# Kernel optimization log

Measured on AMD Instinct MI355X. Metric: run time of the kernel, lower is better.

The kernel has to match this reference:

```python
import jax, jax.numpy as jnp
import numpy as np

B, S, E, H, D = 2, 2048, 1024, 16, 64  # batch, seq(=max_seq_len), embed_dim, heads, atten_dim


def setup_inputs() -> dict:
    key = jax.random.key(0)
    ks = jax.random.split(key, 9)
    s = 0.02
    return {
        "x": jax.random.normal(ks[0], (B, S, E), jnp.float32),
        "Wq": jax.random.normal(ks[1], (H, E, D), jnp.float32) * s,
        "Wk": jax.random.normal(ks[2], (H, E, D), jnp.float32) * s,
        "Wv": jax.random.normal(ks[3], (H, E, D), jnp.float32) * s,
        "bq": jax.random.normal(ks[4], (H, D), jnp.float32) * s,
        "bk": jax.random.normal(ks[5], (H, D), jnp.float32) * s,
        "bv": jax.random.normal(ks[6], (H, D), jnp.float32) * s,
        "Wp": jax.random.normal(ks[7], (H * D, E), jnp.float32) * s,
        "bp": jax.random.normal(ks[8], (E,), jnp.float32) * s,
    }


def reference(x, Wq, Wk, Wv, bq, bk, bv, Wp, bp):
    scale = jnp.sqrt(jnp.float32(D))
    # per-head projections, all heads at once: [B,H,S,D]
    q = jnp.einsum("bse,hed->bhsd", x, Wq) + bq[:, None, :]
    k = jnp.einsum("bse,hed->bhsd", x, Wk) + bk[:, None, :]
    v = jnp.einsum("bse,hed->bhsd", x, Wv) + bv[:, None, :]
    # causal scores [B,H,S,S], additive -inf mask above diagonal (as in the buffer)
    score = jnp.einsum("bhsd,bhtd->bhst", q, k) / scale
    mask = jnp.triu(jnp.full((S, S), -jnp.inf, jnp.float32), k=1)
    score = score + mask
    probs = jax.nn.softmax(score, axis=-1)
    attn = jnp.einsum("bhst,bhtd->bhsd", probs, v)
    # concat heads -> [B,S,H*D], then projection + ReLU
    concat = attn.transpose(0, 2, 1, 3).reshape(B, S, H * D)
    out = jax.nn.relu(concat @ Wp + bp)
    return out
```

## Files before the change

### kernel.cpp

```cpp
#include <hip/hip_runtime.h>

#define S_LEN 2048
#define E_DIM 1024
#define H_NUM 16
#define D_DIM 64

typedef unsigned short u16;
using bf16x8 = __attribute__((ext_vector_type(8))) short;
using f32x4  = __attribute__((ext_vector_type(4))) float;

#define MFMA16(A, B, C) __builtin_amdgcn_mfma_f32_16x16x32_bf16(A, B, C, 0, 0, 0)

__device__ __forceinline__ u16 f2bf(float f) {
    unsigned u = __float_as_uint(f);
    u += 0x7fffu + ((u >> 16) & 1u);
    return (u16)(u >> 16);
}
__device__ __forceinline__ f32x4 fzero4() { f32x4 z; z[0]=0.f; z[1]=0.f; z[2]=0.f; z[3]=0.f; return z; }

__device__ __forceinline__ void gll16(const u16* g, u16* l) {
    __builtin_amdgcn_global_load_lds(
        (const __attribute__((address_space(1))) void*)g,
        (__attribute__((address_space(3))) void*)l, 16, 0, 0);
}

__global__ __launch_bounds__(256) void cvt_bf16(const float* __restrict__ in, u16* __restrict__ outp, int n) {
    int i4 = (blockIdx.x * 256 + threadIdx.x) * 4;
    if (i4 < n) {
        float4 f = *(const float4*)(in + i4);
        unsigned lo = (unsigned)f2bf(f.x) | ((unsigned)f2bf(f.y) << 16);
        unsigned hi = (unsigned)f2bf(f.z) | ((unsigned)f2bf(f.w) << 16);
        uint2 p; p.x = lo; p.y = hi;
        *(uint2*)(outp + i4) = p;
    }
}

__device__ __forceinline__ void cvt_t_tile(const float* __restrict__ bin, u16* __restrict__ bout,
                                           int R, int C, int r0, int c0) {
    __shared__ float t[64][65];
    const int tid = threadIdx.x;
    const int lr = tid >> 2, lc = (tid & 3) * 16;

    const float* src = bin + (size_t)(r0 + lr) * C + c0 + lc;
    #pragma unroll
    for (int j = 0; j < 4; j++) {
        float4 f = *(const float4*)(src + j * 4);
        t[lr][lc + j * 4 + 0] = f.x; t[lr][lc + j * 4 + 1] = f.y;
        t[lr][lc + j * 4 + 2] = f.z; t[lr][lc + j * 4 + 3] = f.w;
    }
    __syncthreads();

    u16* dst = bout + (size_t)(c0 + lr) * R + r0 + lc;
    u16 vals[16];
    #pragma unroll
    for (int i = 0; i < 16; i++) vals[i] = f2bf(t[lc + i][lr]);
    uint4 pa, pb;
    pa.x = vals[0] | (vals[1] << 16);  pa.y = vals[2] | (vals[3] << 16);
    pa.z = vals[4] | (vals[5] << 16);  pa.w = vals[6] | (vals[7] << 16);
    pb.x = vals[8] | (vals[9] << 16);  pb.y = vals[10] | (vals[11] << 16);
    pb.z = vals[12] | (vals[13] << 16); pb.w = vals[14] | (vals[15] << 16);
    *(uint4*)dst = pa;
    *(uint4*)(dst + 8) = pb;
}

__global__ __launch_bounds__(256) void cvt_bf16_t(const float* __restrict__ in, u16* __restrict__ outp,
                                                  int R, int C) {
    const float* bin = in + (size_t)blockIdx.z * R * C;
    u16* bout = outp + (size_t)blockIdx.z * R * C;
    cvt_t_tile(bin, bout, R, C, blockIdx.y * 64, blockIdx.x * 64);
}

__global__ __launch_bounds__(256) void cvt_w3_t(
    const float* __restrict__ Wq, const float* __restrict__ Wk, const float* __restrict__ Wv,
    u16* __restrict__ wqt, u16* __restrict__ wkt, u16* __restrict__ wvt) {
    const int which = blockIdx.z >> 4, bh = blockIdx.z & 15;
    const float* in = (which == 0) ? Wq : (which == 1) ? Wk : Wv;
    u16* outp = (which == 0) ? wqt : (which == 1) ? wkt : wvt;
    const float* bin = in + (size_t)bh * E_DIM * D_DIM;
    u16* bout = outp + (size_t)bh * E_DIM * D_DIM;
    cvt_t_tile(bin, bout, E_DIM, D_DIM, blockIdx.y * 64, 0);
}

__global__ __launch_bounds__(256) void vt_prep(const u16* __restrict__ v, u16* __restrict__ vt) {
    const int st = blockIdx.x;
    const int bhi = blockIdx.y;
    __shared__ u16 t[64 * 72];
    const int tid = threadIdx.x;
    const int wave = tid >> 6, lane = tid & 63;

    const u16* src = v + (size_t)bhi * S_LEN * D_DIM + (size_t)(st * 64 + lane) * D_DIM + wave * 16;
    uint4 a = *(const uint4*)(src);
    uint4 b = *(const uint4*)(src + 8);
    unsigned w[8] = { a.x, a.y, a.z, a.w, b.x, b.y, b.z, b.w };
    #pragma unroll
    for (int j = 0; j < 8; j++) {
        t[(wave * 16 + 2 * j    ) * 72 + lane] = (u16)(w[j] & 0xffffu);
        t[(wave * 16 + 2 * j + 1) * 72 + lane] = (u16)(w[j] >> 16);
    }
    __syncthreads();

    const int dr = tid >> 2, sc = (tid & 3) * 16;
    u16* dst = vt + (size_t)bhi * D_DIM * S_LEN + (size_t)dr * S_LEN + st * 64 + sc;
    *(uint4*)(dst    ) = *(const uint4*)(&t[dr * 72 + sc    ]);
    *(uint4*)(dst + 8) = *(const uint4*)(&t[dr * 72 + sc + 8]);
}

__global__ __launch_bounds__(256) void qkv_gemm(
    const u16* __restrict__ xb, const u16* __restrict__ wcat,
    const float* __restrict__ bq, const float* __restrict__ bk, const float* __restrict__ bv,
    u16* __restrict__ oq, u16* __restrict__ okk, u16* __restrict__ ov)
{
    const int m0 = blockIdx.x * 128;
    const int n0 = blockIdx.y * 128;

    __shared__ u16 As[128 * 32];
    __shared__ u16 Bs[128 * 32];

    const int tid  = threadIdx.x;
    const int wave = tid >> 6, lane = tid & 63, quad = lane >> 4, l16 = lane & 15;
    const int mh = wave >> 1, nh = wave & 1;

    const int lrow = lane >> 2, lcol = (lane & 3) * 8;
    const u16* aBase = xb   + (size_t)(m0 + wave * 32 + lrow) * E_DIM + lcol;
    const u16* bBase = wcat + (size_t)(n0 + wave * 32 + lrow) * E_DIM + lcol;
    u16* aLds0 = &As[(wave * 32     ) * 32];
    u16* aLds1 = &As[(wave * 32 + 16) * 32];
    u16* bLds0 = &Bs[(wave * 32     ) * 32];
    u16* bLds1 = &Bs[(wave * 32 + 16) * 32];

    f32x4 acc[4][4];
    #pragma unroll
    for (int j = 0; j < 4; j++)
        #pragma unroll
        for (int mi = 0; mi < 4; mi++) acc[j][mi] = fzero4();

    for (int k0 = 0; k0 < E_DIM; k0 += 32) {
        __syncthreads();
        gll16(aBase + k0,                 aLds0);
        gll16(aBase + k0 + 16 * E_DIM,    aLds1);
        gll16(bBase + k0,                 bLds0);
        gll16(bBase + k0 + 16 * E_DIM,    bLds1);
        __syncthreads();

        bf16x8 af[4];
        #pragma unroll
        for (int mi = 0; mi < 4; mi++)
            af[mi] = *(const bf16x8*)(&As[(mh * 64 + mi * 16 + l16) * 32 + quad * 8]);
        #pragma unroll
        for (int j = 0; j < 4; j++) {
            bf16x8 bfv = *(const bf16x8*)(&Bs[(nh * 64 + j * 16 + l16) * 32 + quad * 8]);
            #pragma unroll
            for (int mi = 0; mi < 4; mi++)
                acc[j][mi] = MFMA16(af[mi], bfv, acc[j][mi]);
        }
    }

    u16* outp[3] = { oq, okk, ov };
    const float* biasp[3] = { bq, bk, bv };
    #pragma unroll
    for (int j = 0; j < 4; j++) {
        const int n = n0 + nh * 64 + j * 16 + l16;
        const int t = n >> 10, h = (n >> 6) & 15, d = n & 63;
        float bia = biasp[t][h * D_DIM + d];
        const float scl = (t == 0) ? 0.125f : 1.0f;
        u16* dst = outp[t];
        #pragma unroll
        for (int mi = 0; mi < 4; mi++) {
            #pragma unroll
            for (int r = 0; r < 4; r++) {
                int m = m0 + mh * 64 + mi * 16 + quad * 4 + r;
                int b = m >> 11, s = m & 2047;
                dst[((size_t)(b * H_NUM + h) * S_LEN + s) * D_DIM + d] =
                    f2bf((acc[j][mi][r] + bia) * scl);
            }
        }
    }
}

__global__ __launch_bounds__(256) void attn_fwd(
    const u16* __restrict__ q, const u16* __restrict__ k, const u16* __restrict__ vt,
    u16* __restrict__ concat)
{
    const int p  = blockIdx.x;
    const int qa = p, qb = 31 - p;
    const int h  = blockIdx.y;
    const int bb = blockIdx.z;

    const size_t headoff = (size_t)(bb * H_NUM + h) * S_LEN * D_DIM;
    const u16* qh  = q  + headoff;
    const u16* kh  = k  + headoff;
    const u16* vth = vt + headoff;

    __shared__ u16 Qa[64 * 72];
    __shared__ u16 Qb[64 * 72];
    __shared__ u16 Ks[64 * 72];
    __shared__ u16 Vts[64 * 72];
    __shared__ u16 Ps[4][16 * 72];

    const int tid  = threadIdx.x;
    const int wave = tid >> 6, lane = tid & 63, quad = lane >> 4, l16 = lane & 15;

    const int srow = tid >> 2, scg = tid & 3;

    {
        const u16* qsa = qh + (size_t)(qa * 64 + srow) * D_DIM + scg * 16;
        const u16* qsb = qh + (size_t)(qb * 64 + srow) * D_DIM + scg * 16;
        *(uint4*)(&Qa[srow * 72 + scg * 16    ]) = *(const uint4*)(qsa);
        *(uint4*)(&Qa[srow * 72 + scg * 16 + 8]) = *(const uint4*)(qsa + 8);
        *(uint4*)(&Qb[srow * 72 + scg * 16    ]) = *(const uint4*)(qsb);
        *(uint4*)(&Qb[srow * 72 + scg * 16 + 8]) = *(const uint4*)(qsb + 8);
    }
    __syncthreads();

    bf16x8 bqa0 = *(const bf16x8*)(&Qa[(wave * 16 + l16) * 72 + quad * 8]);
    bf16x8 bqa1 = *(const bf16x8*)(&Qa[(wave * 16 + l16) * 72 + 32 + quad * 8]);
    bf16x8 bqb0 = *(const bf16x8*)(&Qb[(wave * 16 + l16) * 72 + quad * 8]);
    bf16x8 bqb1 = *(const bf16x8*)(&Qb[(wave * 16 + l16) * 72 + 32 + quad * 8]);

    f32x4 oa[4], ob[4];
    #pragma unroll
    for (int nt = 0; nt < 4; nt++) { oa[nt] = fzero4(); ob[nt] = fzero4(); }
    float la = 0.f, lb = 0.f;

    uint4 kA, kB, vA, vB;
    {
        const u16* ksrc = kh + (size_t)srow * D_DIM + scg * 16;
        kA = *(const uint4*)(ksrc); kB = *(const uint4*)(ksrc + 8);
        const u16* vsrc = vth + (size_t)srow * S_LEN + scg * 16;
        vA = *(const uint4*)(vsrc); vB = *(const uint4*)(vsrc + 8);
    }

    const int qga = qa * 64 + wave * 16 + l16;
    const int qgb = qb * 64 + wave * 16 + l16;

    for (int kt = 0; kt <= qb; kt++) {
        __syncthreads();
        *(uint4*)(&Ks[srow * 72 + scg * 16    ]) = kA;
        *(uint4*)(&Ks[srow * 72 + scg * 16 + 8]) = kB;
        *(uint4*)(&Vts[srow * 72 + scg * 16    ]) = vA;
        *(uint4*)(&Vts[srow * 72 + scg * 16 + 8]) = vB;
        __syncthreads();

        if (kt < qb) {
            const u16* ksrc = kh + (size_t)((kt + 1) * 64 + srow) * D_DIM + scg * 16;
            kA = *(const uint4*)(ksrc); kB = *(const uint4*)(ksrc + 8);
            const u16* vsrc = vth + (size_t)srow * S_LEN + (kt + 1) * 64 + scg * 16;
            vA = *(const uint4*)(vsrc); vB = *(const uint4*)(vsrc + 8);
        }

        const bool both = (kt <= qa);

        f32x4 stb[4], sta[4];
        #pragma unroll
        for (int nt = 0; nt < 4; nt++) {
            bf16x8 ak0 = *(const bf16x8*)(&Ks[(nt * 16 + l16) * 72 + quad * 8]);
            bf16x8 ak1 = *(const bf16x8*)(&Ks[(nt * 16 + l16) * 72 + 32 + quad * 8]);
            stb[nt] = fzero4();
            stb[nt] = MFMA16(ak0, bqb0, stb[nt]);
            stb[nt] = MFMA16(ak1, bqb1, stb[nt]);
            if (both) {
                sta[nt] = fzero4();
                sta[nt] = MFMA16(ak0, bqa0, sta[nt]);
                sta[nt] = MFMA16(ak1, bqa1, sta[nt]);
            }
        }

        {
            u16* pw = &Ps[wave][0];
            #pragma unroll
            for (int nt = 0; nt < 4; nt++) {
                float pe[4];
                if (kt == qb) {
                    #pragma unroll
                    for (int r = 0; r < 4; r++) {
                        int kkg = kt * 64 + nt * 16 + quad * 4 + r;
                        pe[r] = (kkg > qgb) ? 0.f : __expf(stb[nt][r]);
                    }
                } else {
                    #pragma unroll
                    for (int r = 0; r < 4; r++) pe[r] = __expf(stb[nt][r]);
                }
                lb += pe[0] + pe[1] + pe[2] + pe[3];
                uint2 pk;
                pk.x = (unsigned)f2bf(pe[0]) | ((unsigned)f2bf(pe[1]) << 16);
                pk.y = (unsigned)f2bf(pe[2]) | ((unsigned)f2bf(pe[3]) << 16);
                *(uint2*)(&pw[l16 * 72 + nt * 16 + quad * 4]) = pk;
            }
            bf16x8 ap0 = *(const bf16x8*)(&Ps[wave][l16 * 72 + quad * 8]);
            bf16x8 ap1 = *(const bf16x8*)(&Ps[wave][l16 * 72 + 32 + quad * 8]);
            #pragma unroll
            for (int nt = 0; nt < 4; nt++) {
                bf16x8 bv0 = *(const bf16x8*)(&Vts[(nt * 16 + l16) * 72 + quad * 8]);
                bf16x8 bv1 = *(const bf16x8*)(&Vts[(nt * 16 + l16) * 72 + 32 + quad * 8]);
                ob[nt] = MFMA16(ap0, bv0, ob[nt]);
                ob[nt] = MFMA16(ap1, bv1, ob[nt]);
            }
        }

        if (both) {
            u16* pw = &Ps[wave][0];
            #pragma unroll
            for (int nt = 0; nt < 4; nt++) {
                float pe[4];
                if (kt == qa) {
                    #pragma unroll
                    for (int r = 0; r < 4; r++) {
                        int kkg = kt * 64 + nt * 16 + quad * 4 + r;
                        pe[r] = (kkg > qga) ? 0.f : __expf(sta[nt][r]);
                    }
                } else {
                    #pragma unroll
                    for (int r = 0; r < 4; r++) pe[r] = __expf(sta[nt][r]);
                }
                la += pe[0] + pe[1] + pe[2] + pe[3];
                uint2 pk;
                pk.x = (unsigned)f2bf(pe[0]) | ((unsigned)f2bf(pe[1]) << 16);
                pk.y = (unsigned)f2bf(pe[2]) | ((unsigned)f2bf(pe[3]) << 16);
                *(uint2*)(&pw[l16 * 72 + nt * 16 + quad * 4]) = pk;
            }
            bf16x8 ap0 = *(const bf16x8*)(&Ps[wave][l16 * 72 + quad * 8]);
            bf16x8 ap1 = *(const bf16x8*)(&Ps[wave][l16 * 72 + 32 + quad * 8]);
            #pragma unroll
            for (int nt = 0; nt < 4; nt++) {
                bf16x8 bv0 = *(const bf16x8*)(&Vts[(nt * 16 + l16) * 72 + quad * 8]);
                bf16x8 bv1 = *(const bf16x8*)(&Vts[(nt * 16 + l16) * 72 + 32 + quad * 8]);
                oa[nt] = MFMA16(ap0, bv0, oa[nt]);
                oa[nt] = MFMA16(ap1, bv1, oa[nt]);
            }
        }
    }

    lb += __shfl_xor(lb, 16); lb += __shfl_xor(lb, 32);
    la += __shfl_xor(la, 16); la += __shfl_xor(la, 32);

    #pragma unroll
    for (int r = 0; r < 4; r++) {
        const int srcl = quad * 4 + r;
        float lbr = __shfl(lb, srcl);
        float lar = __shfl(la, srcl);
        int sqa = qa * 64 + wave * 16 + quad * 4 + r;
        int sqb = qb * 64 + wave * 16 + quad * 4 + r;
        #pragma unroll
        for (int nt = 0; nt < 4; nt++) {
            concat[((size_t)(bb * S_LEN + sqa)) * E_DIM + h * D_DIM + nt * 16 + l16] =
                f2bf(oa[nt][r] / lar);
            concat[((size_t)(bb * S_LEN + sqb)) * E_DIM + h * D_DIM + nt * 16 + l16] =
                f2bf(ob[nt][r] / lbr);
        }
    }
}

__global__ __launch_bounds__(256) void out_proj(
    const u16* __restrict__ concat, const u16* __restrict__ wpt,
    const float* __restrict__ bp, float* __restrict__ out)
{
    const int m0 = blockIdx.x * 128;
    const int n0 = blockIdx.y * 128;

    __shared__ u16 As[128 * 40];
    __shared__ u16 Bs[128 * 40];

    const int tid  = threadIdx.x;
    const int wave = tid >> 6, lane = tid & 63, quad = lane >> 4, l16 = lane & 15;
    const int mh = wave >> 1, nh = wave & 1;

    const int arow = tid >> 1, acol = (tid & 1) * 16;

    const u16* aptr = concat + (size_t)(m0 + arow) * E_DIM + acol;
    const u16* bptr = wpt + (size_t)(n0 + arow) * E_DIM + acol;

    f32x4 acc[4][4];
    #pragma unroll
    for (int j = 0; j < 4; j++)
        #pragma unroll
        for (int mi = 0; mi < 4; mi++) acc[j][mi] = fzero4();

    uint4 pA0, pA1, pB0, pB1;
    pA0 = *(const uint4*)(aptr);     pA1 = *(const uint4*)(aptr + 8);
    pB0 = *(const uint4*)(bptr);     pB1 = *(const uint4*)(bptr + 8);

    for (int k0 = 0; k0 < E_DIM; k0 += 32) {
        __syncthreads();
        *(uint4*)(&As[arow * 40 + acol    ]) = pA0;
        *(uint4*)(&As[arow * 40 + acol + 8]) = pA1;
        *(uint4*)(&Bs[arow * 40 + acol    ]) = pB0;
        *(uint4*)(&Bs[arow * 40 + acol + 8]) = pB1;
        __syncthreads();

        if (k0 + 32 < E_DIM) {
            pA0 = *(const uint4*)(aptr + k0 + 32);  pA1 = *(const uint4*)(aptr + k0 + 40);
            pB0 = *(const uint4*)(bptr + k0 + 32);  pB1 = *(const uint4*)(bptr + k0 + 40);
        }

        bf16x8 af[4];
        #pragma unroll
        for (int mi = 0; mi < 4; mi++)
            af[mi] = *(const bf16x8*)(&As[(mh * 64 + mi * 16 + l16) * 40 + quad * 8]);
        #pragma unroll
        for (int j = 0; j < 4; j++) {
            bf16x8 bfv = *(const bf16x8*)(&Bs[(nh * 64 + j * 16 + l16) * 40 + quad * 8]);
            #pragma unroll
            for (int mi = 0; mi < 4; mi++)
                acc[j][mi] = MFMA16(af[mi], bfv, acc[j][mi]);
        }
    }

    #pragma unroll
    for (int j = 0; j < 4; j++) {
        int n = n0 + nh * 64 + j * 16 + l16;
        float bia = bp[n];
        #pragma unroll
        for (int mi = 0; mi < 4; mi++) {
            #pragma unroll
            for (int r = 0; r < 4; r++) {
                int m = m0 + mh * 64 + mi * 16 + quad * 4 + r;
                out[(size_t)m * E_DIM + n] = fmaxf(acc[j][mi][r] + bia, 0.f);
            }
        }
    }
}

extern "C" void kernel_launch(void* const* d_in, const int* in_sizes, int n_in,
                              void* d_out, int out_size, void* d_ws, size_t ws_size,
                              hipStream_t stream)
{
    (void)in_sizes; (void)n_in; (void)out_size; (void)ws_size;
    const float* x  = (const float*)d_in[0];
    const float* Wq = (const float*)d_in[1];
    const float* Wk = (const float*)d_in[2];
    const float* Wv = (const float*)d_in[3];
    const float* bq = (const float*)d_in[4];
    const float* bk = (const float*)d_in[5];
    const float* bv = (const float*)d_in[6];
    const float* Wp = (const float*)d_in[7];
    const float* bp = (const float*)d_in[8];
    float* out = (float*)d_out;

    const size_t QKV_ELEMS = (size_t)2 * H_NUM * S_LEN * D_DIM;
    const size_t W_ELEMS   = (size_t)H_NUM * E_DIM * D_DIM;

    u16* q   = (u16*)d_ws;
    u16* k   = q   + QKV_ELEMS;
    u16* v   = k   + QKV_ELEMS;
    u16* cc  = v   + QKV_ELEMS;
    u16* xb  = cc  + QKV_ELEMS;
    u16* wqt = xb  + QKV_ELEMS;
    u16* wkt = wqt + W_ELEMS;
    u16* wvt = wkt + W_ELEMS;
    u16* wpt = wvt + W_ELEMS;
    u16* vtr = xb;

    cvt_bf16<<<dim3(4096), 256, 0, stream>>>(x, xb, (int)QKV_ELEMS);
    cvt_w3_t<<<dim3(1, 16, 48), 256, 0, stream>>>(Wq, Wk, Wv, wqt, wkt, wvt);
    cvt_bf16_t<<<dim3(16, 16, 1), 256, 0, stream>>>(Wp, wpt, H_NUM * D_DIM, E_DIM);

    qkv_gemm<<<dim3(32, 24), 256, 0, stream>>>(xb, wqt, bq, bk, bv, q, k, v);
    vt_prep<<<dim3(32, 32), 256, 0, stream>>>(v, vtr);
    attn_fwd<<<dim3(16, 16, 2), 256, 0, stream>>>(q, k, vtr, cc);
    out_proj<<<dim3(32, 8), 256, 0, stream>>>(cc, wpt, bp, out);
}
```

Measured before the change: 200.4 us.

## Fuse V transpose into QKV GEMM, double-buffer K/V tiles, use exp2 softmax

The QKV GEMM epilogue now writes V directly in transposed layout, which removes the separate vt_prep kernel and its extra round trip through global memory. The attention kernel double-buffers the K and V shared tiles, so one barrier per iteration is dropped. It also keeps separate P buffers for the two query blocks so the PV MFMAs share the V fragment loads. Q is prescaled by log2(e) so exp2f replaces __expf, and P is packed to bf16 by truncation instead of rounding. The tradeoffs are more LDS use, which may lower occupancy, small precision changes, and transposed V stores that are strided 8-byte writes.

```diff
diff --git a/kernel.cpp b/kernel.cpp
--- a/kernel.cpp
+++ b/kernel.cpp
@@ -15,6 +15,9 @@
     unsigned u = __float_as_uint(f);
     u += 0x7fffu + ((u >> 16) & 1u);
     return (u16)(u >> 16);
+}
+__device__ __forceinline__ unsigned pack_bf16_tr(float lo, float hi) {
+    return (__float_as_uint(lo) >> 16) | (__float_as_uint(hi) & 0xffff0000u);
 }
 __device__ __forceinline__ f32x4 fzero4() { f32x4 z; z[0]=0.f; z[1]=0.f; z[2]=0.f; z[3]=0.f; return z; }
 
@@ -81,34 +84,10 @@
     cvt_t_tile(bin, bout, E_DIM, D_DIM, blockIdx.y * 64, 0);
 }
 
-__global__ __launch_bounds__(256) void vt_prep(const u16* __restrict__ v, u16* __restrict__ vt) {
-    const int st = blockIdx.x;
-    const int bhi = blockIdx.y;
-    __shared__ u16 t[64 * 72];
-    const int tid = threadIdx.x;
-    const int wave = tid >> 6, lane = tid & 63;
-
-    const u16* src = v + (size_t)bhi * S_LEN * D_DIM + (size_t)(st * 64 + lane) * D_DIM + wave * 16;
-    uint4 a = *(const uint4*)(src);
-    uint4 b = *(const uint4*)(src + 8);
-    unsigned w[8] = { a.x, a.y, a.z, a.w, b.x, b.y, b.z, b.w };
-    #pragma unroll
-    for (int j = 0; j < 8; j++) {
-        t[(wave * 16 + 2 * j    ) * 72 + lane] = (u16)(w[j] & 0xffffu);
-        t[(wave * 16 + 2 * j + 1) * 72 + lane] = (u16)(w[j] >> 16);
-    }
-    __syncthreads();
-
-    const int dr = tid >> 2, sc = (tid & 3) * 16;
-    u16* dst = vt + (size_t)bhi * D_DIM * S_LEN + (size_t)dr * S_LEN + st * 64 + sc;
-    *(uint4*)(dst    ) = *(const uint4*)(&t[dr * 72 + sc    ]);
-    *(uint4*)(dst + 8) = *(const uint4*)(&t[dr * 72 + sc + 8]);
-}
-
 __global__ __launch_bounds__(256) void qkv_gemm(
     const u16* __restrict__ xb, const u16* __restrict__ wcat,
     const float* __restrict__ bq, const float* __restrict__ bk, const float* __restrict__ bv,
-    u16* __restrict__ oq, u16* __restrict__ okk, u16* __restrict__ ov)
+    u16* __restrict__ oq, u16* __restrict__ okk, u16* __restrict__ vtr)
 {
     const int m0 = blockIdx.x * 128;
     const int n0 = blockIdx.y * 128;
@@ -155,23 +134,30 @@
         }
     }
 
-    u16* outp[3] = { oq, okk, ov };
-    const float* biasp[3] = { bq, bk, bv };
+    const float QSCL = 0.125f * 1.44269504089f;
     #pragma unroll
     for (int j = 0; j < 4; j++) {
         const int n = n0 + nh * 64 + j * 16 + l16;
         const int t = n >> 10, h = (n >> 6) & 15, d = n & 63;
-        float bia = biasp[t][h * D_DIM + d];
-        const float scl = (t == 0) ? 0.125f : 1.0f;
-        u16* dst = outp[t];
+        const float bia = (t == 0 ? bq : t == 1 ? bk : bv)[h * D_DIM + d];
         #pragma unroll
         for (int mi = 0; mi < 4; mi++) {
-            #pragma unroll
-            for (int r = 0; r < 4; r++) {
-                int m = m0 + mh * 64 + mi * 16 + quad * 4 + r;
-                int b = m >> 11, s = m & 2047;
-                dst[((size_t)(b * H_NUM + h) * S_LEN + s) * D_DIM + d] =
-                    f2bf((acc[j][mi][r] + bia) * scl);
+            const int mbase = m0 + mh * 64 + mi * 16 + quad * 4;
+            const int b = mbase >> 11, s0 = mbase & 2047;
+            if (t == 2) {
+                u16 v0 = f2bf(acc[j][mi][0] + bia), v1 = f2bf(acc[j][mi][1] + bia);
+                u16 v2 = f2bf(acc[j][mi][2] + bia), v3 = f2bf(acc[j][mi][3] + bia);
+                uint2 pk;
+                pk.x = (unsigned)v0 | ((unsigned)v1 << 16);
+                pk.y = (unsigned)v2 | ((unsigned)v3 << 16);
+                *(uint2*)(vtr + ((size_t)(b * H_NUM + h) * D_DIM + d) * S_LEN + s0) = pk;
+            } else {
+                u16* dst = (t == 0) ? oq : okk;
+                const float scl = (t == 0) ? QSCL : 1.0f;
+                #pragma unroll
+                for (int r = 0; r < 4; r++)
+                    dst[((size_t)(b * H_NUM + h) * S_LEN + s0 + r) * D_DIM + d] =
+                        f2bf((acc[j][mi][r] + bia) * scl);
             }
         }
     }
@@ -193,9 +179,10 @@
 
     __shared__ u16 Qa[64 * 72];
     __shared__ u16 Qb[64 * 72];
-    __shared__ u16 Ks[64 * 72];
-    __shared__ u16 Vts[64 * 72];
-    __shared__ u16 Ps[4][16 * 72];
+    __shared__ u16 Ks[2][64 * 72];
+    __shared__ u16 Vts[2][64 * 72];
+    __shared__ u16 Psa[4][16 * 72];
+    __shared__ u16 Psb[4][16 * 72];
 
     const int tid  = threadIdx.x;
     const int wave = tid >> 6, lane = tid & 63, quad = lane >> 4, l16 = lane & 15;
@@ -234,11 +221,12 @@
     const int qgb = qb * 64 + wave * 16 + l16;
 
     for (int kt = 0; kt <= qb; kt++) {
-        __syncthreads();
-        *(uint4*)(&Ks[srow * 72 + scg * 16    ]) = kA;
-        *(uint4*)(&Ks[srow * 72 + scg * 16 + 8]) = kB;
-        *(uint4*)(&Vts[srow * 72 + scg * 16    ]) = vA;
-        *(uint4*)(&Vts[srow * 72 + scg * 16 + 8]) = vB;
+        u16* ksb = &Ks[kt & 1][0];
+        u16* vsb = &Vts[kt & 1][0];
+        *(uint4*)(&ksb[srow * 72 + scg * 16    ]) = kA;
+        *(uint4*)(&ksb[srow * 72 + scg * 16 + 8]) = kB;
+        *(uint4*)(&vsb[srow * 72 + scg * 16    ]) = vA;
+        *(uint4*)(&vsb[srow * 72 + scg * 16 + 8]) = vB;
         __syncthreads();
 
         if (kt < qb) {
@@ -253,8 +241,8 @@
         f32x4 stb[4], sta[4];
         #pragma unroll
         for (int nt = 0; nt < 4; nt++) {
-            bf16x8 ak0 = *(const bf16x8*)(&Ks[(nt * 16 + l16) * 72 + quad * 8]);
-            bf16x8 ak1 = *(const bf16x8*)(&Ks[(nt * 16 + l16) * 72 + 32 + quad * 8]);
+            bf16x8 ak0 = *(const bf16x8*)(&ksb[(nt * 16 + l16) * 72 + quad * 8]);
+            bf16x8 ak1 = *(const bf16x8*)(&ksb[(nt * 16 + l16) * 72 + 32 + quad * 8]);
             stb[nt] = fzero4();
             stb[nt] = MFMA16(ak0, bqb0, stb[nt]);
             stb[nt] = MFMA16(ak1, bqb1, stb[nt]);
@@ -266,7 +254,7 @@
         }
 
         {
-            u16* pw = &Ps[wave][0];
+            u16* pw = &Psb[wave][0];
             #pragma unroll
             for (int nt = 0; nt < 4; nt++) {
                 float pe[4];
@@ -274,31 +262,21 @@
                     #pragma unroll
                     for (int r = 0; r < 4; r++) {
                         int kkg = kt * 64 + nt * 16 + quad * 4 + r;
-                        pe[r] = (kkg > qgb) ? 0.f : __expf(stb[nt][r]);
+                        pe[r] = (kkg > qgb) ? 0.f : exp2f(stb[nt][r]);
                     }
                 } else {
                     #pragma unroll
-                    for (int r = 0; r < 4; r++) pe[r] = __expf(stb[nt][r]);
+                    for (int r = 0; r < 4; r++) pe[r] = exp2f(stb[nt][r]);
                 }
                 lb += pe[0] + pe[1] + pe[2] + pe[3];
                 uint2 pk;
-                pk.x = (unsigned)f2bf(pe[0]) | ((unsigned)f2bf(pe[1]) << 16);
-                pk.y = (unsigned)f2bf(pe[2]) | ((unsigned)f2bf(pe[3]) << 16);
+                pk.x = pack_bf16_tr(pe[0], pe[1]);
+                pk.y = pack_bf16_tr(pe[2], pe[3]);
                 *(uint2*)(&pw[l16 * 72 + nt * 16 + quad * 4]) = pk;
             }
-            bf16x8 ap0 = *(const bf16x8*)(&Ps[wave][l16 * 72 + quad * 8]);
-            bf16x8 ap1 = *(const bf16x8*)(&Ps[wave][l16 * 72 + 32 + quad * 8]);
-            #pragma unroll
-            for (int nt = 0; nt < 4; nt++) {
-                bf16x8 bv0 = *(const bf16x8*)(&Vts[(nt * 16 + l16) * 72 + quad * 8]);
-                bf16x8 bv1 = *(const bf16x8*)(&Vts[(nt * 16 + l16) * 72 + 32 + quad * 8]);
-                ob[nt] = MFMA16(ap0, bv0, ob[nt]);
-                ob[nt] = MFMA16(ap1, bv1, ob[nt]);
-            }
-        }
-
+        }
         if (both) {
-            u16* pw = &Ps[wave][0];
+            u16* pw = &Psa[wave][0];
             #pragma unroll
             for (int nt = 0; nt < 4; nt++) {
                 float pe[4];
@@ -306,26 +284,38 @@
                     #pragma unroll
                     for (int r = 0; r < 4; r++) {
                         int kkg = kt * 64 + nt * 16 + quad * 4 + r;
-                        pe[r] = (kkg > qga) ? 0.f : __expf(sta[nt][r]);
+                        pe[r] = (kkg > qga) ? 0.f : exp2f(sta[nt][r]);
                     }
                 } else {
                     #pragma unroll
-                    for (int r = 0; r < 4; r++) pe[r] = __expf(sta[nt][r]);
+                    for (int r = 0; r < 4; r++) pe[r] = exp2f(sta[nt][r]);
                 }
                 la += pe[0] + pe[1] + pe[2] + pe[3];
                 uint2 pk;
-                pk.x = (unsigned)f2bf(pe[0]) | ((unsigned)f2bf(pe[1]) << 16);
-                pk.y = (unsigned)f2bf(pe[2]) | ((unsigned)f2bf(pe[3]) << 16);
+                pk.x = pack_bf16_tr(pe[0], pe[1]);
+                pk.y = pack_bf16_tr(pe[2], pe[3]);
                 *(uint2*)(&pw[l16 * 72 + nt * 16 + quad * 4]) = pk;
             }
-            bf16x8 ap0 = *(const bf16x8*)(&Ps[wave][l16 * 72 + quad * 8]);
-            bf16x8 ap1 = *(const bf16x8*)(&Ps[wave][l16 * 72 + 32 + quad * 8]);
+        }
+
+        {
+            bf16x8 apb0 = *(const bf16x8*)(&Psb[wave][l16 * 72 + quad * 8]);
+            bf16x8 apb1 = *(const bf16x8*)(&Psb[wave][l16 * 72 + 32 + quad * 8]);
+            bf16x8 apa0, apa1;
+            if (both) {
+                apa0 = *(const bf16x8*)(&Psa[wave][l16 * 72 + quad * 8]);
+                apa1 = *(const bf16x8*)(&Psa[wave][l16 * 72 + 32 + quad * 8]);
+            }
             #pragma unroll
             for (int nt = 0; nt < 4; nt++) {
-                bf16x8 bv0 = *(const bf16x8*)(&Vts[(nt * 16 + l16) * 72 + quad * 8]);
-                bf16x8 bv1 = *(const bf16x8*)(&Vts[(nt * 16 + l16) * 72 + 32 + quad * 8]);
-                oa[nt] = MFMA16(ap0, bv0, oa[nt]);
-                oa[nt] = MFMA16(ap1, bv1, oa[nt]);
+                bf16x8 bv0 = *(const bf16x8*)(&vsb[(nt * 16 + l16) * 72 + quad * 8]);
+                bf16x8 bv1 = *(const bf16x8*)(&vsb[(nt * 16 + l16) * 72 + 32 + quad * 8]);
+                ob[nt] = MFMA16(apb0, bv0, ob[nt]);
+                ob[nt] = MFMA16(apb1, bv1, ob[nt]);
+                if (both) {
+                    oa[nt] = MFMA16(apa0, bv0, oa[nt]);
+                    oa[nt] = MFMA16(apa1, bv1, oa[nt]);
+                }
             }
         }
     }
@@ -441,21 +431,19 @@
 
     u16* q   = (u16*)d_ws;
     u16* k   = q   + QKV_ELEMS;
-    u16* v   = k   + QKV_ELEMS;
-    u16* cc  = v   + QKV_ELEMS;
+    u16* vtr = k   + QKV_ELEMS;
+    u16* cc  = vtr + QKV_ELEMS;
     u16* xb  = cc  + QKV_ELEMS;
     u16* wqt = xb  + QKV_ELEMS;
     u16* wkt = wqt + W_ELEMS;
     u16* wvt = wkt + W_ELEMS;
     u16* wpt = wvt + W_ELEMS;
-    u16* vtr = xb;
 
     cvt_bf16<<<dim3(4096), 256, 0, stream>>>(x, xb, (int)QKV_ELEMS);
     cvt_w3_t<<<dim3(1, 16, 48), 256, 0, stream>>>(Wq, Wk, Wv, wqt, wkt, wvt);
     cvt_bf16_t<<<dim3(16, 16, 1), 256, 0, stream>>>(Wp, wpt, H_NUM * D_DIM, E_DIM);
 
-    qkv_gemm<<<dim3(32, 24), 256, 0, stream>>>(xb, wqt, bq, bk, bv, q, k, v);
-    vt_prep<<<dim3(32, 32), 256, 0, stream>>>(v, vtr);
+    qkv_gemm<<<dim3(32, 24), 256, 0, stream>>>(xb, wqt, bq, bk, bv, q, k, vtr);
     attn_fwd<<<dim3(16, 16, 2), 256, 0, stream>>>(q, k, vtr, cc);
     out_proj<<<dim3(32, 8), 256, 0, stream>>>(cc, wpt, bp, out);
 }
```

Measured after the change: 213.1 us. 6.3% more time.
